# Kernel tuning notes

Measured on AMD Instinct MI355X. Metric: run time of the kernel, lower is better.

The kernel has to match this reference:

```python
import jax, jax.numpy as jnp
import numpy as np
import math

GRID = 32          # config.grid_size
DIM = 256          # sparse_head_dim = n_embd * mlp_internal_dim_multiplier // n_head
B, H = 8, 8        # batch, n_head
N = GRID * GRID    # tokens = grid_size^2


def get_freqs_2d(h, w, dim, theta=10000.0):
    """2D RoPE angles; returns (cos, sin) each of shape (h*w, dim//2)."""
    dim_half = dim // 2
    inv = 1.0 / theta ** (np.arange(0, dim_half, 2).astype(np.float32) / dim_half)
    fx = np.outer(np.arange(w, dtype=np.float32), inv)   # (w, dim_half//2)
    fy = np.outer(np.arange(h, dtype=np.float32), inv)   # (h, dim_half//2)
    fx_grid = np.broadcast_to(fx[None, :, :], (h, w, fx.shape[1]))
    fy_grid = np.broadcast_to(fy[:, None, :], (h, w, fy.shape[1]))
    ang = np.concatenate([fx_grid, fy_grid], axis=-1).reshape(h * w, dim_half)
    return jnp.asarray(np.cos(ang)), jnp.asarray(np.sin(ang))


def apply_rotary(x, cos, sin):
    # x: (B,H,N,D) viewed as complex pairs along last dim; complex multiply by e^{i*ang}
    xr = x.reshape(*x.shape[:-1], -1, 2)
    x0, x1 = xr[..., 0], xr[..., 1]          # (B,H,N,D/2)
    out_re = x0 * cos - x1 * sin
    out_im = x0 * sin + x1 * cos
    return jnp.stack([out_re, out_im], axis=-1).reshape(x.shape)


def setup_inputs() -> dict:
    key = jax.random.key(0)
    k1, k2, k3 = jax.random.split(key, 3)
    shape = (B, H, N, DIM)
    return {
        "Q": jax.random.normal(k1, shape, dtype=jnp.float32),
        "K": jax.random.normal(k2, shape, dtype=jnp.float32),
        "V": jax.random.normal(k3, shape, dtype=jnp.float32),
    }


def reference(Q, K, V):
    cos, sin = get_freqs_2d(GRID, GRID, DIM)  # (N, DIM/2) each, broadcast over B,H
    QR = apply_rotary(Q, cos, sin)
    KR = apply_rotary(K, cos, sin)
    scores = jnp.einsum('bhnd,bhmd->bhnm', QR, KR) / math.sqrt(QR.shape[-1])
    attn = jax.nn.softmax(scores, axis=-1)
    return jnp.einsum('bhnm,bhmd->bhnd', attn, V)
```

## Files before the change

### kernel.cpp

```cpp
#include <hip/hip_runtime.h>
#include <hip/hip_bf16.h>
#include <cstdint>

#define BH     64
#define NTOK   1024
#define DDIM   256
#define QT     128
#define KTILE  32
#define NITER  (NTOK / KTILE)

typedef __bf16 bf16x8 __attribute__((ext_vector_type(8)));
typedef float  f32x16 __attribute__((ext_vector_type(16)));

__device__ __forceinline__ unsigned short f2bf(float f) {
    __bf16 b = (__bf16)f;
    return __builtin_bit_cast(unsigned short, b);
}
__device__ __forceinline__ float bf2f(unsigned short u) {
    return __builtin_bit_cast(float, ((unsigned int)u) << 16);
}
__device__ __forceinline__ unsigned int pack2(float lo, float hi) {
    return (unsigned int)f2bf(lo) | ((unsigned int)f2bf(hi) << 16);
}

__device__ __forceinline__ void sincos_rev(float rev, float* s, float* c) {
    float fr = rev - __builtin_floorf(rev);
    *s = __builtin_amdgcn_sinf(fr);
    *c = __builtin_amdgcn_cosf(fr);
}

typedef const __attribute__((address_space(1))) unsigned int* gas_t;
typedef __attribute__((address_space(3))) unsigned int* las_t;
__device__ __forceinline__ void gload16(const void* g, void* l) {
    __builtin_amdgcn_global_load_lds((gas_t)g, (las_t)l, 16, 0, 0);
}

#define ANG_C    (13.287712379549449f / 64.0f)
#define L2_2PI   2.6514961294723187f
#define SM_SCALE (1.4426950408889634f / 16.0f)

__global__ __launch_bounds__(256) void prep(const float* __restrict__ K,
                                            const float* __restrict__ V,
                                            unsigned short* __restrict__ KR,
                                            unsigned short* __restrict__ VT) {
    __shared__ unsigned short tile[64 * 264];
    int tid = threadIdx.x;
    if (blockIdx.x < 8192) {
        int gid = blockIdx.x * 256 + tid;
        int chunk = gid & 31;
        int t = (gid >> 5) & (NTOK - 1);
        float x = (float)(t & 31), y = (float)(t >> 5);
        const float4 a = *(const float4*)(K + (size_t)gid * 8);
        const float4 b = *(const float4*)(K + (size_t)gid * 8 + 4);
        float f[8] = {a.x, a.y, a.z, a.w, b.x, b.y, b.z, b.w};
        unsigned int o[4];
#pragma unroll
        for (int p = 0; p < 4; ++p) {
            int j = chunk * 4 + p;
            float pos = (j < 64) ? x : y;
            float invr = __builtin_exp2f(-(float)(j & 63) * ANG_C - L2_2PI);
            float s, c;
            sincos_rev(pos * invr, &s, &c);
            float x0 = f[2 * p], x1 = f[2 * p + 1];
            o[p] = pack2(x0 * c - x1 * s, x0 * s + x1 * c);
        }
        uint4 ov; ov.x = o[0]; ov.y = o[1]; ov.z = o[2]; ov.w = o[3];
        *(uint4*)(KR + (size_t)gid * 8) = ov;
        return;
    }
    int vb = blockIdx.x - 8192;
    int bh = vb >> 4;
    int tbase = (vb & 15) * 64;
    const float* src = V + ((size_t)bh * NTOK + tbase) * DDIM;
#pragma unroll
    for (int i = 0; i < 8; ++i) {
        int flat = i * 2048 + tid * 8;
        int tl = flat >> 8, col = flat & 255;
        const float4 a = *(const float4*)(src + (size_t)tl * DDIM + col);
        const float4 b = *(const float4*)(src + (size_t)tl * DDIM + col + 4);
        uint4 ov;
        ov.x = pack2(a.x, a.y); ov.y = pack2(a.z, a.w);
        ov.z = pack2(b.x, b.y); ov.w = pack2(b.z, b.w);
        *(uint4*)(tile + tl * 264 + col) = ov;
    }
    __syncthreads();
    unsigned short* dst = VT + (size_t)bh * ((size_t)DDIM * NTOK) + tbase;
#pragma unroll
    for (int i = 0; i < 8; ++i) {
        int task = i * 256 + tid;
        int d = task >> 3, tq = task & 7;
        unsigned int o[4];
#pragma unroll
        for (int k = 0; k < 4; ++k) {
            unsigned short lo = tile[(tq * 8 + 2 * k    ) * 264 + d];
            unsigned short hi = tile[(tq * 8 + 2 * k + 1) * 264 + d];
            o[k] = (unsigned int)lo | ((unsigned int)hi << 16);
        }
        uint4 ov; ov.x = o[0]; ov.y = o[1]; ov.z = o[2]; ov.w = o[3];
        *(uint4*)(dst + (size_t)d * NTOK + tq * 8) = ov;
    }
}

__global__ __launch_bounds__(256, 2) void flash_attn(
        const float* __restrict__ Q,
        const unsigned short* __restrict__ KR,
        const unsigned short* __restrict__ VTg,
        float* __restrict__ Out) {
    __shared__ unsigned short KT[2][KTILE * DDIM];
    __shared__ unsigned short VTl[2][DDIM * KTILE];

    const int tid = threadIdx.x;
    const int wave = tid >> 6, lane = tid & 63;
    const int l31 = lane & 31, h = lane >> 5;
    const int b = blockIdx.x;
    const int bh = (b & 7) + ((b >> 6) << 3);
    const int qbase = ((b >> 3) & 7) * QT;

    const unsigned short* krB = KR + (size_t)bh * ((size_t)NTOK * DDIM);
    const unsigned short* vtB = VTg + (size_t)bh * ((size_t)DDIM * NTOK);

    bf16x8 qfrag[16];
    {
        const int qtok = qbase + wave * 32 + l31;
        const float x = (float)(qtok & 31), y = (float)(qtok >> 5);
        const float* qrow = Q + ((size_t)bh * NTOK + qtok) * DDIM;
#pragma unroll
        for (int cc = 0; cc < 16; ++cc) {
            const float4 a = *(const float4*)(qrow + cc * 16 + h * 8);
            const float4 b2 = *(const float4*)(qrow + cc * 16 + h * 8 + 4);
            float f[8] = {a.x, a.y, a.z, a.w, b2.x, b2.y, b2.z, b2.w};
            unsigned int po[4];
#pragma unroll
            for (int p = 0; p < 4; ++p) {
                int j = cc * 8 + h * 4 + p;
                float pos = (j < 64) ? x : y;
                float invr = __builtin_exp2f(-(float)(j & 63) * ANG_C - L2_2PI);
                float s, c;
                sincos_rev(pos * invr, &s, &c);
                float x0 = f[2 * p], x1 = f[2 * p + 1];
                po[p] = pack2(x0 * c - x1 * s, x0 * s + x1 * c);
            }
            uint4 pk; pk.x = po[0]; pk.y = po[1]; pk.z = po[2]; pk.w = po[3];
            qfrag[cc] = __builtin_bit_cast(bf16x8, pk);
        }
    }
    asm volatile("s_waitcnt vmcnt(0)" ::: "memory");

    f32x16 o[8] = {};
    float lsum[4] = {};

    int kOff[4], vOff[4];
#pragma unroll
    for (int j = 0; j < 4; ++j) {
        int f = wave * 256 + j * 64 + lane;
        int rf = f >> 5, sf = f & 31;
        kOff[j] = rf * 256 + ((sf ^ (rf & 7)) * 8);
        int gI = f ^ ((f >> 3) & 3);
        vOff[j] = (gI >> 2) * NTOK + (gI & 3) * 8;
    }
    const int kx = l31 & 7;
    const int vx = (l31 >> 1) & 3;
    const int vbase = l31 * 32;
    const int vh0 = (h ^ vx) * 8;
    const int vh1 = ((2 + h) ^ vx) * 8;

#pragma unroll
    for (int j = 0; j < 4; ++j)
        gload16(krB + kOff[j], &KT[0][wave * 2048 + j * 512]);
#pragma unroll
    for (int j = 0; j < 4; ++j)
        gload16(vtB + vOff[j], &VTl[0][wave * 2048 + j * 512]);

    for (int it = 0; it < NITER; ++it) {
        const int cur = it & 1;
        if (it + 1 < NITER) {
            const int kb = (it + 1) * KTILE;
            const unsigned short* krT = krB + (size_t)kb * DDIM;
            const unsigned short* vtT = vtB + kb;
            const int nxt = cur ^ 1;
#pragma unroll
            for (int j = 0; j < 4; ++j)
                gload16(krT + kOff[j], &KT[nxt][wave * 2048 + j * 512]);
#pragma unroll
            for (int j = 0; j < 4; ++j)
                gload16(vtT + vOff[j], &VTl[nxt][wave * 2048 + j * 512]);
            asm volatile("s_waitcnt vmcnt(8)" ::: "memory");
        } else {
            asm volatile("s_waitcnt vmcnt(0)" ::: "memory");
        }
        __builtin_amdgcn_s_barrier();

        f32x16 sc = {};
        const unsigned short* ktb = KT[cur];
        __builtin_amdgcn_s_setprio(1);
#pragma unroll
        for (int cc = 0; cc < 16; ++cc) {
            const int sl = ((2 * cc + h) ^ kx) * 8;
            bf16x8 kb_ = *(const bf16x8*)(ktb + l31 * 256 + sl);
            sc = __builtin_amdgcn_mfma_f32_32x32x16_bf16(kb_, qfrag[cc], sc, 0, 0, 0);
        }
        __builtin_amdgcn_s_setprio(0);

        unsigned short bs[16];
#pragma unroll
        for (int r = 0; r < 16; ++r) {
            float p = __builtin_exp2f(sc[r] * SM_SCALE);
            bs[r] = f2bf(p);
            lsum[r & 3] += bf2f(bs[r]);
        }
        bf16x8 pa[2];
#pragma unroll
        for (int c = 0; c < 2; ++c) {
            unsigned int P1 = (unsigned)bs[c*8+0] | ((unsigned)bs[c*8+1] << 16);
            unsigned int P2 = (unsigned)bs[c*8+2] | ((unsigned)bs[c*8+3] << 16);
            unsigned int P3 = (unsigned)bs[c*8+4] | ((unsigned)bs[c*8+5] << 16);
            unsigned int P4 = (unsigned)bs[c*8+6] | ((unsigned)bs[c*8+7] << 16);
            unsigned int P1x = __shfl_xor((int)P1, 32);
            unsigned int P2x = __shfl_xor((int)P2, 32);
            unsigned int P3x = __shfl_xor((int)P3, 32);
            unsigned int P4x = __shfl_xor((int)P4, 32);
            uint4 w;
            w.x = h ? P3x : P1;
            w.y = h ? P4x : P2;
            w.z = h ? P3  : P1x;
            w.w = h ? P4  : P2x;
            pa[c] = __builtin_bit_cast(bf16x8, w);
        }

        const unsigned short* vtb = VTl[cur];
        __builtin_amdgcn_s_setprio(1);
#pragma unroll
        for (int nt = 0; nt < 8; ++nt) {
            const unsigned short* vp = vtb + nt * 1024 + vbase;
            bf16x8 v0 = *(const bf16x8*)(vp + vh0);
            bf16x8 v1 = *(const bf16x8*)(vp + vh1);
            o[nt] = __builtin_amdgcn_mfma_f32_32x32x16_bf16(pa[0], v0, o[nt], 0, 0, 0);
            o[nt] = __builtin_amdgcn_mfma_f32_32x32x16_bf16(pa[1], v1, o[nt], 0, 0, 0);
        }
        __builtin_amdgcn_s_setprio(0);

        asm volatile("s_waitcnt lgkmcnt(0)" ::: "memory");
        __builtin_amdgcn_s_barrier();
    }

    float tot = (lsum[0] + lsum[1]) + (lsum[2] + lsum[3]);
    tot += __shfl_xor(tot, 32);
#pragma unroll
    for (int r = 0; r < 16; ++r) {
        const int q = (r & 3) + 8 * (r >> 2) + 4 * h;
        float rl = 1.0f / __shfl(tot, q);
        float* orow =
            Out + ((size_t)bh * NTOK + qbase + wave * 32 + q) * DDIM;
#pragma unroll
        for (int nt = 0; nt < 8; ++nt)
            orow[nt * 32 + l31] = o[nt][r] * rl;
    }
}

extern "C" void kernel_launch(void* const* d_in, const int* in_sizes, int n_in,
                              void* d_out, int out_size, void* d_ws, size_t ws_size,
                              hipStream_t stream) {
    const float* Q = (const float*)d_in[0];
    const float* K = (const float*)d_in[1];
    const float* V = (const float*)d_in[2];
    unsigned short* KR = (unsigned short*)d_ws;
    unsigned short* VT = KR + (size_t)BH * NTOK * DDIM;
    float* O = (float*)d_out;

    prep<<<8192 + BH * (NTOK / 64), 256, 0, stream>>>(K, V, KR, VT);
    flash_attn<<<BH * (NTOK / QT), 256, 0, stream>>>(Q, KR, VT, O);
}
```

Before: 309.0 us.

## Stage K/V tiles through registers instead of direct global-to-LDS loads

Replaces the global_load_lds async copies with ordinary global loads into registers that are written to LDS after compute. Loads are issued two tiles ahead and the swizzle moves from the global side to the LDS write side. The QK^T MFMA chain is split into two independent accumulators to shorten the dependency chain, and the s_setprio hints are removed. This costs extra VGPRs for the staging buffers and adds explicit LDS write instructions, which may hurt occupancy at launch_bounds(256,2).

```diff
diff --git a/kernel.cpp b/kernel.cpp
--- a/kernel.cpp
+++ b/kernel.cpp
@@ -27,12 +27,6 @@
     float fr = rev - __builtin_floorf(rev);
     *s = __builtin_amdgcn_sinf(fr);
     *c = __builtin_amdgcn_cosf(fr);
-}
-
-typedef const __attribute__((address_space(1))) unsigned int* gas_t;
-typedef __attribute__((address_space(3))) unsigned int* las_t;
-__device__ __forceinline__ void gload16(const void* g, void* l) {
-    __builtin_amdgcn_global_load_lds((gas_t)g, (las_t)l, 16, 0, 0);
 }
 
 #define ANG_C    (13.287712379549449f / 64.0f)
@@ -119,6 +113,23 @@
     const unsigned short* krB = KR + (size_t)bh * ((size_t)NTOK * DDIM);
     const unsigned short* vtB = VTg + (size_t)bh * ((size_t)DDIM * NTOK);
 
+    int kG[4], vG[4], kL[4], vL[4];
+#pragma unroll
+    for (int j = 0; j < 4; ++j) {
+        int f = wave * 256 + j * 64 + lane;
+        kG[j] = f * 8;
+        vG[j] = (f >> 2) * NTOK + (f & 3) * 8;
+        int rf = f >> 5, sf = f & 31;
+        kL[j] = rf * 256 + ((sf ^ (rf & 7)) * 8);
+        vL[j] = (f ^ ((f >> 3) & 3)) * 8;
+    }
+
+    uint4 kst[4], vst[4];
+#pragma unroll
+    for (int j = 0; j < 4; ++j) kst[j] = *(const uint4*)(krB + kG[j]);
+#pragma unroll
+    for (int j = 0; j < 4; ++j) vst[j] = *(const uint4*)(vtB + vG[j]);
+
     bf16x8 qfrag[16];
     {
         const int qtok = qbase + wave * 32 + l31;
@@ -144,62 +155,43 @@
             qfrag[cc] = __builtin_bit_cast(bf16x8, pk);
         }
     }
-    asm volatile("s_waitcnt vmcnt(0)" ::: "memory");
 
     f32x16 o[8] = {};
     float lsum[4] = {};
 
-    int kOff[4], vOff[4];
-#pragma unroll
-    for (int j = 0; j < 4; ++j) {
-        int f = wave * 256 + j * 64 + lane;
-        int rf = f >> 5, sf = f & 31;
-        kOff[j] = rf * 256 + ((sf ^ (rf & 7)) * 8);
-        int gI = f ^ ((f >> 3) & 3);
-        vOff[j] = (gI >> 2) * NTOK + (gI & 3) * 8;
-    }
     const int kx = l31 & 7;
     const int vx = (l31 >> 1) & 3;
     const int vbase = l31 * 32;
     const int vh0 = (h ^ vx) * 8;
     const int vh1 = ((2 + h) ^ vx) * 8;
 
-#pragma unroll
-    for (int j = 0; j < 4; ++j)
-        gload16(krB + kOff[j], &KT[0][wave * 2048 + j * 512]);
-#pragma unroll
-    for (int j = 0; j < 4; ++j)
-        gload16(vtB + vOff[j], &VTl[0][wave * 2048 + j * 512]);
+    asm volatile("s_waitcnt vmcnt(0)" ::: "memory");
+#pragma unroll
+    for (int j = 0; j < 4; ++j) *(uint4*)(&KT[0][kL[j]]) = kst[j];
+#pragma unroll
+    for (int j = 0; j < 4; ++j) *(uint4*)(&VTl[0][vL[j]]) = vst[j];
+#pragma unroll
+    for (int j = 0; j < 4; ++j) kst[j] = *(const uint4*)(krB + KTILE * DDIM + kG[j]);
+#pragma unroll
+    for (int j = 0; j < 4; ++j) vst[j] = *(const uint4*)(vtB + KTILE + vG[j]);
+    asm volatile("s_waitcnt lgkmcnt(0)" ::: "memory");
+    __builtin_amdgcn_s_barrier();
 
     for (int it = 0; it < NITER; ++it) {
         const int cur = it & 1;
-        if (it + 1 < NITER) {
-            const int kb = (it + 1) * KTILE;
-            const unsigned short* krT = krB + (size_t)kb * DDIM;
-            const unsigned short* vtT = vtB + kb;
-            const int nxt = cur ^ 1;
-#pragma unroll
-            for (int j = 0; j < 4; ++j)
-                gload16(krT + kOff[j], &KT[nxt][wave * 2048 + j * 512]);
-#pragma unroll
-            for (int j = 0; j < 4; ++j)
-                gload16(vtT + vOff[j], &VTl[nxt][wave * 2048 + j * 512]);
-            asm volatile("s_waitcnt vmcnt(8)" ::: "memory");
-        } else {
-            asm volatile("s_waitcnt vmcnt(0)" ::: "memory");
-        }
-        __builtin_amdgcn_s_barrier();
-
-        f32x16 sc = {};
+
+        f32x16 sca = {}, scb = {};
         const unsigned short* ktb = KT[cur];
-        __builtin_amdgcn_s_setprio(1);
-#pragma unroll
-        for (int cc = 0; cc < 16; ++cc) {
-            const int sl = ((2 * cc + h) ^ kx) * 8;
-            bf16x8 kb_ = *(const bf16x8*)(ktb + l31 * 256 + sl);
-            sc = __builtin_amdgcn_mfma_f32_32x32x16_bf16(kb_, qfrag[cc], sc, 0, 0, 0);
-        }
-        __builtin_amdgcn_s_setprio(0);
+#pragma unroll
+        for (int cc = 0; cc < 8; ++cc) {
+            const int sla = ((2 * cc + h) ^ kx) * 8;
+            const int slb = ((2 * (cc + 8) + h) ^ kx) * 8;
+            bf16x8 ka = *(const bf16x8*)(ktb + l31 * 256 + sla);
+            bf16x8 kb_ = *(const bf16x8*)(ktb + l31 * 256 + slb);
+            sca = __builtin_amdgcn_mfma_f32_32x32x16_bf16(ka, qfrag[cc], sca, 0, 0, 0);
+            scb = __builtin_amdgcn_mfma_f32_32x32x16_bf16(kb_, qfrag[cc + 8], scb, 0, 0, 0);
+        }
+        f32x16 sc = sca + scb;
 
         unsigned short bs[16];
 #pragma unroll
@@ -228,7 +220,6 @@
         }
 
         const unsigned short* vtb = VTl[cur];
-        __builtin_amdgcn_s_setprio(1);
 #pragma unroll
         for (int nt = 0; nt < 8; ++nt) {
             const unsigned short* vp = vtb + nt * 1024 + vbase;
@@ -237,10 +228,26 @@
             o[nt] = __builtin_amdgcn_mfma_f32_32x32x16_bf16(pa[0], v0, o[nt], 0, 0, 0);
             o[nt] = __builtin_amdgcn_mfma_f32_32x32x16_bf16(pa[1], v1, o[nt], 0, 0, 0);
         }
-        __builtin_amdgcn_s_setprio(0);
-
-        asm volatile("s_waitcnt lgkmcnt(0)" ::: "memory");
-        __builtin_amdgcn_s_barrier();
+
+        if (it + 1 < NITER) {
+            const int nxt = cur ^ 1;
+            asm volatile("s_waitcnt vmcnt(0)" ::: "memory");
+#pragma unroll
+            for (int j = 0; j < 4; ++j) *(uint4*)(&KT[nxt][kL[j]]) = kst[j];
+#pragma unroll
+            for (int j = 0; j < 4; ++j) *(uint4*)(&VTl[nxt][vL[j]]) = vst[j];
+            if (it + 2 < NITER) {
+                const int kb2 = (it + 2) * KTILE;
+#pragma unroll
+                for (int j = 0; j < 4; ++j)
+                    kst[j] = *(const uint4*)(krB + kb2 * DDIM + kG[j]);
+#pragma unroll
+                for (int j = 0; j < 4; ++j)
+                    vst[j] = *(const uint4*)(vtB + kb2 + vG[j]);
+            }
+            asm volatile("s_waitcnt lgkmcnt(0)" ::: "memory");
+            __builtin_amdgcn_s_barrier();
+        }
     }
 
     float tot = (lsum[0] + lsum[1]) + (lsum[2] + lsum[3]);
```

After: 499.8 us. 1.62x slower.
